# Kernel tuning notes

Hardware: AMD Instinct MI355X
Metric: run time of the kernel (lower is better)

Reference implementation:

```python
import jax, jax.numpy as jnp
import numpy as np

CODEBOOK_SIZE = 8192
EMBED_DIM = 256


def setup_inputs() -> dict:
    key = jax.random.key(0)
    k1, k2 = jax.random.split(key)
    z_e = jax.random.normal(k1, (16, EMBED_DIM, 32, 32), dtype=jnp.float32)
    # nn.init.uniform_(weight, -1/K, 1/K)
    embed_weight = jax.random.uniform(
        k2, (CODEBOOK_SIZE, EMBED_DIM), dtype=jnp.float32,
        minval=-1.0 / CODEBOOK_SIZE, maxval=1.0 / CODEBOOK_SIZE)
    return {"z_e": z_e, "embed_weight": embed_weight}


def reference(z_e, embed_weight):
    # euclidean metric -> projections are identity; z_metric == z_e
    B, C, H, W = z_e.shape
    K = embed_weight.shape[0]
    z_flat = z_e.transpose(0, 2, 3, 1).reshape(-1, C)  # [N, D], N = B*H*W
    # squared euclidean distances: ||z||^2 + ||e||^2 - 2 z e^T  -> [N, K]
    distances = ((z_flat * z_flat).sum(axis=1, keepdims=True)
                 + (embed_weight * embed_weight).sum(axis=1)[None, :]
                 - 2.0 * jnp.matmul(z_flat, embed_weight.T))
    codes_flat = jnp.argmin(distances, axis=1)  # [N]
    z_q = embed_weight[codes_flat].reshape(B, H, W, C).transpose(0, 3, 1, 2)  # [B,C,H,W]
    # straight-through estimator
    z_q_st = z_e + jax.lax.stop_gradient(z_q - z_e)
    # eval / non-EMA path: both losses are MSE
    codebook_loss = jnp.mean(jnp.square(z_q - jax.lax.stop_gradient(z_e)))
    commitment_loss = jnp.mean(jnp.square(z_e - jax.lax.stop_gradient(z_q)))
    # usage statistics
    code_counts = jnp.bincount(codes_flat, length=K).astype(z_e.dtype)
    avg_probs = code_counts / jnp.maximum(code_counts.sum(), 1.0)
    perplexity = jnp.exp(-jnp.sum(avg_probs * jnp.log(jnp.maximum(avg_probs, 1e-10))))
    used_code_count = (code_counts > 0).sum().astype(z_e.dtype)
    used_code_fraction = used_code_count / float(K)
    dead_code_fraction = 1.0 - used_code_fraction
    return (z_q_st, jax.lax.stop_gradient(z_q), codes_flat.reshape(B, H, W),
            codebook_loss, commitment_loss, perplexity,
            used_code_count, used_code_fraction, dead_code_fraction)
```

## Files before the change

kernel.cpp:

```cpp
#include <hip/hip_runtime.h>

typedef __attribute__((ext_vector_type(8))) short bf16x8;
typedef __attribute__((ext_vector_type(4))) float f32x4;

#define D_DIM 256
#define K_CODES 8192
#define N_TOK 16384
#define MARGIN 2.5e-4f
#define CAP 96
#define LCAP 24
#define FILT_Q 200u
#define QSCALE 1638400.0f
#define QOFF 0.02f

__device__ __forceinline__ float pw128_sq(const float* a, int stride) {
    float r[8];
    #pragma unroll
    for (int j = 0; j < 8; ++j) { float v = a[j * stride]; r[j] = __fmul_rn(v, v); }
    for (int i = 8; i < 128; i += 8) {
        #pragma unroll
        for (int j = 0; j < 8; ++j) { float v = a[(i + j) * stride]; r[j] = __fadd_rn(r[j], __fmul_rn(v, v)); }
    }
    return __fadd_rn(__fadd_rn(__fadd_rn(r[0], r[1]), __fadd_rn(r[2], r[3])),
                     __fadd_rn(__fadd_rn(r[4], r[5]), __fadd_rn(r[6], r[7])));
}
__device__ __forceinline__ float sumsq256(const float* a, int stride) {
    return __fadd_rn(pw128_sq(a, stride), pw128_sq(a + 128 * stride, stride));
}

__device__ __forceinline__ unsigned f2bf_u(float f) {
    unsigned u = __float_as_uint(f);
    return (u + 0x7FFFu + ((u >> 16) & 1u)) >> 16;
}

__global__ __launch_bounds__(256) void enorm_kernel(const float* __restrict__ embed,
                                                    float* __restrict__ e_norm) {
    int code = blockIdx.x * 256 + threadIdx.x;
    e_norm[code] = sumsq256(embed + code * D_DIM, 1);
}

__global__ __launch_bounds__(256) void znorm_kernel(const float* __restrict__ z_e,
                                                    float* __restrict__ z_norm) {
    int n = blockIdx.x * 256 + threadIdx.x;
    int b = n >> 10, hw = n & 1023;
    z_norm[n] = sumsq256(z_e + b * 262144 + hw, 1024);
}

__global__ __launch_bounds__(256) void ecvt_kernel(const float* __restrict__ embed,
                                                   ushort* __restrict__ e_bf) {
    int i = blockIdx.x * 256 + threadIdx.x;
    float4 v = reinterpret_cast<const float4*>(embed)[i];
    ushort4 o;
    o.x = (ushort)f2bf_u(v.x); o.y = (ushort)f2bf_u(v.y);
    o.z = (ushort)f2bf_u(v.z); o.w = (ushort)f2bf_u(v.w);
    reinterpret_cast<ushort4*>(e_bf)[i] = o;
}

__global__ __launch_bounds__(256, 4) void mfma_argmin_kernel(
    const float* __restrict__ z_e, const ushort* __restrict__ e_bf,
    const float* __restrict__ e_norm,
    unsigned* __restrict__ ccount, unsigned* __restrict__ cand)
{
    __shared__ char zs[32768];
    __shared__ unsigned cand_l[64][LCAP];
    __shared__ unsigned cnt_l[64];

    const int tid = threadIdx.x;
    const int l   = tid & 63;
    const int wv  = tid >> 6;
    const int col = l & 15;
    const int kg  = l >> 4;
    const int bid = (int)blockIdx.x;
    const int slab= (bid >> 1) & 3;
    const int mb  = ((bid >> 3) << 1) | (bid & 1);
    const int n0  = mb * 64;
    const int bb  = n0 >> 10;
    const int hw0 = n0 & 1023;
    const int cs  = slab * 2048 + wv * 512;

    if (tid < 64) { cnt_l[tid] = 0; cand_l[tid][LCAP - 1] = 0xFFFFFFFFu; }

    {
        const float* zb = z_e + bb * 262144 + hw0 + l;
        int swz = (l & 7) << 4;
        #pragma unroll 4
        for (int it = 0; it < 32; ++it) {
            int d = it * 8 + wv * 2;
            float a0 = zb[d * 1024];
            float a1 = zb[d * 1024 + 1024];
            unsigned pk = f2bf_u(a0) | (f2bf_u(a1) << 16);
            *(unsigned*)(zs + l * 512 + ((d * 2) ^ swz)) = pk;
        }
    }
    __syncthreads();

    const int a_swz = (col & 7) << 4;
    const char* bbase = (const char*)e_bf + (size_t)(cs + col) * 512 + kg * 16;
    const float* enb = e_norm + cs + col;

    float runmin[4][4];
    #pragma unroll
    for (int i0 = 0; i0 < 4; ++i0)
        #pragma unroll
        for (int i1 = 0; i1 < 4; ++i1) runmin[i0][i1] = 3.4e38f;

    f32x4 acc[4][4];
    bf16x8 bA[4], bB[4];

    #define LDB(dst, step) { int _t = (step) >> 3, _kb = (step) & 7;                         \
        _Pragma("unroll")                                                                    \
        for (int nt = 0; nt < 4; ++nt)                                                       \
            dst[nt] = *(const bf16x8*)(bbase + _t * 32768 + nt * 8192 + _kb * 64); }

    #define COMPUTE(bf, step) {                                                              \
        int _kb = (step) & 7;                                                                \
        if (_kb == 0) {                                                                      \
            _Pragma("unroll")                                                                \
            for (int rt = 0; rt < 4; ++rt)                                                   \
                _Pragma("unroll")                                                            \
                for (int nt = 0; nt < 4; ++nt) acc[rt][nt] = f32x4{0.f, 0.f, 0.f, 0.f};      \
        }                                                                                    \
        int a_off = (_kb * 64 + kg * 16) ^ a_swz;                                            \
        _Pragma("unroll")                                                                    \
        for (int rt = 0; rt < 4; ++rt) {                                                     \
            bf16x8 afr = *(const bf16x8*)(zs + (rt * 16 + col) * 512 + a_off);               \
            _Pragma("unroll")                                                                \
            for (int nt = 0; nt < 4; ++nt)                                                   \
                acc[rt][nt] = __builtin_amdgcn_mfma_f32_16x16x32_bf16(afr, bf[nt], acc[rt][nt], 0, 0, 0); \
        }                                                                                    \
        if (_kb == 7) {                                                                      \
            int _t = (step) >> 3;                                                            \
            int cb = cs + _t * 64;                                                           \
            float en[4];                                                                     \
            _Pragma("unroll")                                                                \
            for (int nt = 0; nt < 4; ++nt) en[nt] = enb[_t * 64 + nt * 16];                  \
            _Pragma("unroll")                                                                \
            for (int rt = 0; rt < 4; ++rt)                                                   \
                _Pragma("unroll")                                                            \
                for (int nt = 0; nt < 4; ++nt)                                               \
                    _Pragma("unroll")                                                        \
                    for (int r = 0; r < 4; ++r)                                              \
                        acc[rt][nt][r] = fmaf(-2.0f, acc[rt][nt][r], en[nt]);                \
            _Pragma("unroll")                                                                \
            for (int rt = 0; rt < 4; ++rt) {                                                 \
                _Pragma("unroll")                                                            \
                for (int r = 0; r < 4; ++r) {                                                \
                    float m4 = fminf(fminf(acc[rt][0][r], acc[rt][1][r]),                    \
                                     fminf(acc[rt][2][r], acc[rt][3][r]));                   \
                    float tm = m4;                                                           \
                    tm = fminf(tm, __shfl_xor(tm, 1, 64));                                   \
                    tm = fminf(tm, __shfl_xor(tm, 2, 64));                                   \
                    tm = fminf(tm, __shfl_xor(tm, 4, 64));                                   \
                    tm = fminf(tm, __shfl_xor(tm, 8, 64));                                   \
                    float rm = fminf(runmin[rt][r], tm);                                     \
                    runmin[rt][r] = rm;                                                      \
                    float thr = rm + MARGIN;                                                 \
                    if (m4 < thr) {                                                          \
                        int tl = rt * 16 + kg * 4 + r;                \
                        _Pragma("unroll")                                                    \
                        for (int nt2 = 0; nt2 < 4; ++nt2) {                                  \
                            float s = acc[rt][nt2][r];                                       \
                            if (s < thr) {                                                   \
                                int q = (int)((s + QOFF) * QSCALE);                          \
                                q = q < 0 ? 0 : (q > 65535 ? 65535 : q);                     \
                                unsigned w = ((unsigned)q << 16)                             \
                                           | (unsigned)(cb + nt2 * 16 + col);                \
                                unsigned p = atomicAdd(&cnt_l[tl], 1u);      \
                                if (p < LCAP - 1) cand_l[tl][p] = w;                         \
                                else atomicMin(&cand_l[tl][LCAP - 1], w);                    \
                            }                                                                \
                        }                                                                    \
                    }                                                                        \
                }                                                                            \
            }                                                                                \
        }                                                                                    \
    }

    LDB(bA, 0);
    for (int sp = 0; sp < 32; ++sp) {
        int step = sp * 2;
        LDB(bB, step + 1);
        COMPUTE(bA, step);
        if (step + 2 < 64) LDB(bA, step + 2);
        COMPUTE(bB, step + 1);
    }
    #undef LDB
    #undef COMPUTE

    __syncthreads();
    if (tid < 64) {
        unsigned cl = cnt_l[tid]; if (cl > LCAP) cl = LCAP;
        if (cl) {
            int token = n0 + tid;
            unsigned p = atomicAdd(&ccount[token], cl);
            for (unsigned i = 0; i < cl && p + i < CAP; ++i)
                cand[token * CAP + p + i] = cand_l[tid][i];
        }
    }
}

__global__ __launch_bounds__(256) void rescore_kernel(
    const float* __restrict__ z_e, const float* __restrict__ embed,
    const float* __restrict__ e_norm, const float* __restrict__ z_norm,
    const unsigned* __restrict__ ccount, const unsigned* __restrict__ cand,
    int* __restrict__ codes, float* __restrict__ out, int* __restrict__ counts)
{
    __shared__ float zrow[4][256];
    int wv = threadIdx.x >> 6, l = threadIdx.x & 63;
    int n = blockIdx.x * 4 + wv;
    int b = n >> 10, hw = n & 1023;
    const float* zb = z_e + b * 262144 + hw;
    #pragma unroll
    for (int j = 0; j < 4; ++j) zrow[wv][l * 4 + j] = zb[(l * 4 + j) * 1024];
    __syncthreads();

    unsigned cnt = ccount[n]; if (cnt > CAP) cnt = CAP;
    unsigned c0 = ((unsigned)l      < cnt) ? cand[n * CAP + l]      : 0xFFFFFFFFu;
    unsigned c1 = ((unsigned)l + 64 < cnt) ? cand[n * CAP + l + 64] : 0xFFFFFFFFu;
    unsigned qm = min(c0 >> 16, c1 >> 16);
    #pragma unroll
    for (int m = 1; m < 64; m <<= 1) qm = min(qm, (unsigned)__shfl_xor((int)qm, m, 64));
    unsigned qthr = qm + FILT_Q;

    float best = 3.4e38f; int bidx = 0x7FFFFFFF;
    float zn = z_norm[n];
    #pragma unroll
    for (int pass = 0; pass < 2; ++pass) {
        unsigned cd = pass ? c1 : c0;
        if ((cd >> 16) <= qthr) {
            int idx = (int)(cd & 0xFFFFu);
            const float* er = embed + idx * D_DIM;
            float dot = 0.f;
            for (int d = 0; d < 256; d += 4) {
                float4 e4 = *reinterpret_cast<const float4*>(er + d);
                dot = fmaf(zrow[wv][d],     e4.x, dot);
                dot = fmaf(zrow[wv][d + 1], e4.y, dot);
                dot = fmaf(zrow[wv][d + 2], e4.z, dot);
                dot = fmaf(zrow[wv][d + 3], e4.w, dot);
            }
            float s = __fsub_rn(__fadd_rn(zn, e_norm[idx]), __fmul_rn(2.0f, dot));
            if (s < best || (s == best && idx < bidx)) { best = s; bidx = idx; }
        }
    }
    #pragma unroll
    for (int m = 1; m < 64; m <<= 1) {
        float s2 = __shfl_xor(best, m, 64);
        int   i2 = __shfl_xor(bidx, m, 64);
        if (s2 < best || (s2 == best && i2 < bidx)) { best = s2; bidx = i2; }
    }
    if (l == 0) {
        codes[n] = bidx;
        out[8388608 + n] = (float)bidx;
        atomicAdd(&counts[bidx], 1);
    }
}

__global__ __launch_bounds__(256) void gather_kernel(const float* __restrict__ z_e,
                                                     const float* __restrict__ embed,
                                                     const int* __restrict__ codes,
                                                     float* __restrict__ out,
                                                     float* __restrict__ loss_sum) {
    __shared__ float zq[32][257];
    __shared__ int cds[32];
    const int tid = threadIdx.x;
    const int n0 = blockIdx.x * 32;
    if (tid < 32) cds[tid] = codes[n0 + tid];
    __syncthreads();
    #pragma unroll 4
    for (int it = 0; it < 32; ++it)
        zq[it][tid] = embed[cds[it] * D_DIM + tid];
    __syncthreads();

    const int bb = n0 >> 10, hw0 = n0 & 1023;
    const int n32 = tid & 31, dl = tid >> 5;
    float sq = 0.f;
    #pragma unroll 4
    for (int it = 0; it < 32; ++it) {
        int d = it * 8 + dl;
        float v = zq[n32][d];
        int pos = (bb * 256 + d) * 1024 + hw0 + n32;
        out[pos] = v;
        out[4194304 + pos] = v;
        float df = v - z_e[pos];
        sq = fmaf(df, df, sq);
    }
    #pragma unroll
    for (int m = 1; m < 64; m <<= 1) sq += __shfl_xor(sq, m, 64);
    __shared__ float wsum[4];
    if ((tid & 63) == 0) wsum[tid >> 6] = sq;
    __syncthreads();
    if (tid == 0) atomicAdd(loss_sum, wsum[0] + wsum[1] + wsum[2] + wsum[3]);
}

__global__ __launch_bounds__(256) void stats_kernel(const int* __restrict__ counts,
                                                    const float* __restrict__ loss_sum,
                                                    float* __restrict__ out) {
    __shared__ double Hs[256];
    __shared__ int us[256];
    double H = 0.0; int used = 0;
    for (int k = threadIdx.x; k < K_CODES; k += 256) {
        int cnt = counts[k];
        if (cnt > 0) { double p = (double)cnt / 16384.0; H -= p * log(p); ++used; }
    }
    Hs[threadIdx.x] = H; us[threadIdx.x] = used;
    __syncthreads();
    for (int s = 128; s > 0; s >>= 1) {
        if (threadIdx.x < s) { Hs[threadIdx.x] += Hs[threadIdx.x + s]; us[threadIdx.x] += us[threadIdx.x + s]; }
        __syncthreads();
    }
    if (threadIdx.x == 0) {
        float loss = loss_sum[0] / 4194304.0f;
        float usedf = (float)us[0];
        out[8404992 + 0] = loss;
        out[8404992 + 1] = loss;
        out[8404992 + 2] = (float)exp(Hs[0]);
        out[8404992 + 3] = usedf;
        out[8404992 + 4] = usedf / 8192.0f;
        out[8404992 + 5] = 1.0f - usedf / 8192.0f;
    }
}

extern "C" void kernel_launch(void* const* d_in, const int* in_sizes, int n_in,
                              void* d_out, int out_size, void* d_ws, size_t ws_size,
                              hipStream_t stream) {
    const float* z_e   = (const float*)d_in[0];
    const float* embed = (const float*)d_in[1];
    float* out = (float*)d_out;
    float* ws  = (float*)d_ws;

    float*    e_norm   = ws;
    float*    z_norm   = ws + 8192;
    int*      codes    = (int*)(ws + 24576);
    int*      counts   = (int*)(ws + 40960);
    float*    loss_sum = ws + 49152;
    unsigned* ccount   = (unsigned*)(ws + 49408);
    unsigned* cand     = (unsigned*)(ws + 65792);
    ushort*   e_bf     = (ushort*)(ws + 1638656);

    hipMemsetAsync(counts, 0, 8193 * sizeof(int), stream);
    hipMemsetAsync(ccount, 0, 16384 * sizeof(unsigned), stream);

    enorm_kernel<<<32, 256, 0, stream>>>(embed, e_norm);
    znorm_kernel<<<64, 256, 0, stream>>>(z_e, z_norm);
    ecvt_kernel<<<2048, 256, 0, stream>>>(embed, e_bf);
    mfma_argmin_kernel<<<1024, 256, 0, stream>>>(z_e, e_bf, e_norm, ccount, cand);
    rescore_kernel<<<4096, 256, 0, stream>>>(z_e, embed, e_norm, z_norm, ccount, cand, codes, out, counts);
    gather_kernel<<<512, 256, 0, stream>>>(z_e, embed, codes, out, loss_sum);
    stats_kernel<<<1, 256, 0, stream>>>(counts, loss_sum, out);
}
```

Before: 286.3 us.

## Fuse prep kernels and memsets, deepen B prefetch, vectorize rescore z load

Merges the bf16 conversion, codebook norm and token norm kernels plus the two memsets into one prep launch, and parallelises the codebook norm across 16 lanes per code with shuffle reductions. The MFMA argmin loop now keeps four B-fragment register buffers in flight instead of two, and its occupancy hint drops from 4 to 3 blocks per CU to make room for the extra registers. The rescore kernel loads four adjacent tokens' z values with one float4 per thread instead of strided scalar loads. These aim to cut launch overhead and global-load latency, at the cost of higher register pressure and fewer resident waves in the main kernel.

Measured after the change: 307.8 us. +7.5%, slower.

```diff
diff --git a/kernel.cpp b/kernel.cpp
--- a/kernel.cpp
+++ b/kernel.cpp
@@ -33,30 +33,45 @@
     return (u + 0x7FFFu + ((u >> 16) & 1u)) >> 16;
 }
 
-__global__ __launch_bounds__(256) void enorm_kernel(const float* __restrict__ embed,
-                                                    float* __restrict__ e_norm) {
-    int code = blockIdx.x * 256 + threadIdx.x;
-    e_norm[code] = sumsq256(embed + code * D_DIM, 1);
-}
-
-__global__ __launch_bounds__(256) void znorm_kernel(const float* __restrict__ z_e,
-                                                    float* __restrict__ z_norm) {
-    int n = blockIdx.x * 256 + threadIdx.x;
-    int b = n >> 10, hw = n & 1023;
-    z_norm[n] = sumsq256(z_e + b * 262144 + hw, 1024);
-}
-
-__global__ __launch_bounds__(256) void ecvt_kernel(const float* __restrict__ embed,
-                                                   ushort* __restrict__ e_bf) {
-    int i = blockIdx.x * 256 + threadIdx.x;
-    float4 v = reinterpret_cast<const float4*>(embed)[i];
-    ushort4 o;
-    o.x = (ushort)f2bf_u(v.x); o.y = (ushort)f2bf_u(v.y);
-    o.z = (ushort)f2bf_u(v.z); o.w = (ushort)f2bf_u(v.w);
-    reinterpret_cast<ushort4*>(e_bf)[i] = o;
-}
-
-__global__ __launch_bounds__(256, 4) void mfma_argmin_kernel(
+__global__ __launch_bounds__(256) void prep_kernel(const float* __restrict__ z_e,
+                                                   const float* __restrict__ embed,
+                                                   float* __restrict__ e_norm,
+                                                   float* __restrict__ z_norm,
+                                                   ushort* __restrict__ e_bf,
+                                                   unsigned* __restrict__ ccount,
+                                                   int* __restrict__ counts) {
+    int bid = blockIdx.x;
+    if (bid < 2048) {
+        int i = bid * 256 + threadIdx.x;
+        float4 v = reinterpret_cast<const float4*>(embed)[i];
+        ushort4 o;
+        o.x = (ushort)f2bf_u(v.x); o.y = (ushort)f2bf_u(v.y);
+        o.z = (ushort)f2bf_u(v.z); o.w = (ushort)f2bf_u(v.w);
+        reinterpret_cast<ushort4*>(e_bf)[i] = o;
+    } else if (bid < 2560) {
+        int tid = threadIdx.x;
+        int code = (bid - 2048) * 16 + (tid >> 4);
+        int sub = tid & 15;
+        const float* base = embed + code * 256 + (sub >> 3) * 128 + (sub & 7);
+        float v = base[0];
+        float r = __fmul_rn(v, v);
+        #pragma unroll
+        for (int i = 8; i < 128; i += 8) { v = base[i]; r = __fadd_rn(r, __fmul_rn(v, v)); }
+        r = __fadd_rn(r, __shfl_xor(r, 1, 64));
+        r = __fadd_rn(r, __shfl_xor(r, 2, 64));
+        r = __fadd_rn(r, __shfl_xor(r, 4, 64));
+        r = __fadd_rn(r, __shfl_xor(r, 8, 64));
+        if (sub == 0) e_norm[code] = r;
+    } else {
+        int n = (bid - 2560) * 256 + threadIdx.x;
+        int b = n >> 10, hw = n & 1023;
+        z_norm[n] = sumsq256(z_e + b * 262144 + hw, 1024);
+        ccount[n] = 0;
+        if (n < 8193) counts[n] = 0;
+    }
+}
+
+__global__ __launch_bounds__(256, 3) void mfma_argmin_kernel(
     const float* __restrict__ z_e, const ushort* __restrict__ e_bf,
     const float* __restrict__ e_norm,
     unsigned* __restrict__ ccount, unsigned* __restrict__ cand)
@@ -105,7 +120,7 @@
         for (int i1 = 0; i1 < 4; ++i1) runmin[i0][i1] = 3.4e38f;
 
     f32x4 acc[4][4];
-    bf16x8 bA[4], bB[4];
+    bf16x8 b0[4], b1[4], b2[4], b3[4];
 
     #define LDB(dst, step) { int _t = (step) >> 3, _kb = (step) & 7;                         \
         _Pragma("unroll")                                                                    \
@@ -176,13 +191,13 @@
         }                                                                                    \
     }
 
-    LDB(bA, 0);
-    for (int sp = 0; sp < 32; ++sp) {
-        int step = sp * 2;
-        LDB(bB, step + 1);
-        COMPUTE(bA, step);
-        if (step + 2 < 64) LDB(bA, step + 2);
-        COMPUTE(bB, step + 1);
+    LDB(b0, 0); LDB(b1, 1); LDB(b2, 2);
+    for (int sp = 0; sp < 16; ++sp) {
+        int s = sp * 4;
+        LDB(b3, s + 3);        COMPUTE(b0, s);
+        LDB(b0, (s + 4) & 63); COMPUTE(b1, s + 1);
+        LDB(b1, (s + 5) & 63); COMPUTE(b2, s + 2);
+        LDB(b2, (s + 6) & 63); COMPUTE(b3, s + 3);
     }
     #undef LDB
     #undef COMPUTE
@@ -208,10 +223,13 @@
     __shared__ float zrow[4][256];
     int wv = threadIdx.x >> 6, l = threadIdx.x & 63;
     int n = blockIdx.x * 4 + wv;
-    int b = n >> 10, hw = n & 1023;
-    const float* zb = z_e + b * 262144 + hw;
-    #pragma unroll
-    for (int j = 0; j < 4; ++j) zrow[wv][l * 4 + j] = zb[(l * 4 + j) * 1024];
+    {
+        int n0 = blockIdx.x * 4;
+        int b = n0 >> 10, hw0 = n0 & 1023;
+        float4 v = *reinterpret_cast<const float4*>(z_e + b * 262144 + threadIdx.x * 1024 + hw0);
+        zrow[0][threadIdx.x] = v.x; zrow[1][threadIdx.x] = v.y;
+        zrow[2][threadIdx.x] = v.z; zrow[3][threadIdx.x] = v.w;
+    }
     __syncthreads();
 
     unsigned cnt = ccount[n]; if (cnt > CAP) cnt = CAP;
@@ -337,12 +355,7 @@
     unsigned* cand     = (unsigned*)(ws + 65792);
     ushort*   e_bf     = (ushort*)(ws + 1638656);
 
-    hipMemsetAsync(counts, 0, 8193 * sizeof(int), stream);
-    hipMemsetAsync(ccount, 0, 16384 * sizeof(unsigned), stream);
-
-    enorm_kernel<<<32, 256, 0, stream>>>(embed, e_norm);
-    znorm_kernel<<<64, 256, 0, stream>>>(z_e, z_norm);
-    ecvt_kernel<<<2048, 256, 0, stream>>>(embed, e_bf);
+    prep_kernel<<<2624, 256, 0, stream>>>(z_e, embed, e_norm, z_norm, e_bf, ccount, counts);
     mfma_argmin_kernel<<<1024, 256, 0, stream>>>(z_e, e_bf, e_norm, ccount, cand);
     rescore_kernel<<<4096, 256, 0, stream>>>(z_e, embed, e_norm, z_norm, ccount, cand, codes, out, counts);
     gather_kernel<<<512, 256, 0, stream>>>(z_e, embed, codes, out, loss_sum);
```
